# Performance work log

Measured on AMD Instinct MI355X. Metric: run time of the kernel, lower is better.

## Reference

```python
import jax, jax.numpy as jnp
import numpy as np
from math import factorial as _f

MAX_L = 2
NUM_CHANNELS = 64
B, N, C = 4, 1024, 64


def _cg_coeff(l1, m1, l2, m2, L, M):
    # Standard real Clebsch-Gordan coefficient <l1 m1 l2 m2 | L M> (Condon-Shortley)
    if m1 + m2 != M or not (abs(l1 - l2) <= L <= l1 + l2):
        return 0.0
    pre = ((2 * L + 1) * _f(L + l1 - l2) * _f(L - l1 + l2) * _f(l1 + l2 - L) / _f(l1 + l2 + L + 1)) ** 0.5
    pre *= (_f(L + M) * _f(L - M) * _f(l1 - m1) * _f(l1 + m1) * _f(l2 - m2) * _f(l2 + m2)) ** 0.5
    s = 0.0
    for k in range(0, l1 + l2 - L + 1):
        dens = [k, l1 + l2 - L - k, l1 - m1 - k, l2 + m2 - k, L - l2 + m1 + k, L - l1 - m2 + k]
        if any(d < 0 for d in dens):
            continue
        term = (-1.0) ** k
        for d in dens:
            term /= _f(d)
        s += term
    return pre * s


def _cg_tensor(l1, l2, L):
    # dense CG block [2l1+1, 2l2+1, 2L+1]
    T = np.zeros((2 * l1 + 1, 2 * l2 + 1, 2 * L + 1), np.float32)
    for i, m1 in enumerate(range(-l1, l1 + 1)):
        for j, m2 in enumerate(range(-l2, l2 + 1)):
            for k, M in enumerate(range(-L, L + 1)):
                T[i, j, k] = _cg_coeff(l1, m1, l2, m2, L, M)
    return jnp.asarray(T)


# precompute small CG blocks once (tiny, static)
_CG = {(l1, l2, L): _cg_tensor(l1, l2, L)
       for l1 in range(MAX_L + 1) for l2 in range(MAX_L + 1)
       for L in range(MAX_L + 1) if abs(l1 - l2) <= L <= l1 + l2}


def setup_inputs() -> dict:
    key = jax.random.key(0)
    ks = jax.random.split(key, 7)
    inp = {}
    for l, k in zip(range(MAX_L + 1), ks[:3]):
        inp[f"v{l}"] = jax.random.normal(k, (B, N, 2 * l + 1, C), jnp.float32)
    for l, k in zip(range(MAX_L + 1), ks[3:6]):
        inp[f"s{l}"] = jax.random.normal(k, (B, N, N, 2 * l + 1, 1), jnp.float32)
    inp["conn"] = jax.random.randint(ks[6], (B, N, N), 0, 2, jnp.int32)
    return inp


def reference(v0, v1, v2, s0, s1, s2, conn):
    v = [v0, v1, v2]
    sph = [s0, s1, s2]
    # sphx.parts[l] = einsum('bijmc->bimc', sph.parts[l]) : sum over neighbor index j
    sx = [jnp.einsum('bijmc->bimc', s) for s in sph]
    adj = conn.astype(v0.dtype)  # [B,N,N] gather mask (Rmask1)

    # CGproduct(vertices, sphx): for each output degree L, concat all (l1,l2) fragments
    cg_parts = []
    for L in range(MAX_L + 1):
        frags = []
        for l1 in range(MAX_L + 1):
            for l2 in range(MAX_L + 1):
                if abs(l1 - l2) <= L <= l1 + l2:
                    # [B,N,2L+1,C*1]
                    o = jnp.einsum('bnic,bnjd,ijk->bnkcd', v[l1], sx[l2], _CG[(l1, l2, L)])
                    frags.append(o.reshape(o.shape[0], o.shape[1], 2 * L + 1, -1))
        cg_parts.append(jnp.concatenate(frags, axis=-1))

    # message passing: sum-gather over connected neighbors
    mp = [jnp.einsum('bnm,bmkc->bnkc', adj, p) for p in cg_parts]

    # per-l normalization: divide by (2l+1)*||part||_F / num_channels
    normed = []
    for L, p in enumerate(mp):
        nf = (2 * L + 1) * jnp.linalg.norm(p)
        normed.append(p / (nf / NUM_CHANNELS))

    # flatten (m, channel) per degree and concat for a single output array
    return jnp.concatenate([p.reshape(p.shape[0], p.shape[1], -1) for p in normed], axis=-1)
```

## Files before the change

kernel.cpp:

```cpp
#include <hip/hip_runtime.h>
#include <math.h>

typedef __attribute__((ext_vector_type(8))) short short8;
typedef __attribute__((ext_vector_type(4))) float f32x4;

#define B_   4
#define N_   1024
#define FTOT 3264
#define FPAD 3328

#define WS_SS   0
#define WS_CG   256
#define WS_SX   4096
#define WS_ABF  151552
#define WS_PT   8540160

__device__ __forceinline__ unsigned short f2bf(float x) {
  union { float f; unsigned u; } v; v.f = x;
  unsigned r = v.u + 0x7FFFu + ((v.u >> 16) & 1u);
  return (unsigned short)(r >> 16);
}

__device__ __forceinline__ void gload16(const void* gp, void* lp) {
  __builtin_amdgcn_global_load_lds((const __attribute__((address_space(1))) unsigned int*)gp,
                                   (__attribute__((address_space(3))) unsigned int*)lp, 16, 0, 0);
}

__device__ __forceinline__ float wave_sum(float v) {
#pragma unroll
  for (int off = 32; off > 0; off >>= 1) v += __shfl_down(v, off, 64);
  return v;
}

__device__ double dfact(int n) { double r = 1.0; for (int i = 2; i <= n; ++i) r *= (double)i; return r; }

__device__ float cg_coeff(int l1, int m1, int l2, int m2, int L, int M) {
  if (m1 + m2 != M) return 0.f;
  int dl = l1 - l2; if (dl < 0) dl = -dl;
  if (L < dl || L > l1 + l2) return 0.f;
  double pre = sqrt((double)(2*L+1) * dfact(L+l1-l2) * dfact(L-l1+l2) * dfact(l1+l2-L) / dfact(l1+l2+L+1));
  pre *= sqrt(dfact(L+M)*dfact(L-M)*dfact(l1-m1)*dfact(l1+m1)*dfact(l2-m2)*dfact(l2+m2));
  double s = 0.0;
  for (int k = 0; k <= l1 + l2 - L; ++k) {
    int d1 = l1+l2-L-k, d2 = l1-m1-k, d3 = l2+m2-k, d4 = L-l2+m1+k, d5 = L-l1-m2+k;
    if (d1 < 0 || d2 < 0 || d3 < 0 || d4 < 0 || d5 < 0) continue;
    double t = (k & 1) ? -1.0 : 1.0;
    t /= dfact(k)*dfact(d1)*dfact(d2)*dfact(d3)*dfact(d4)*dfact(d5);
    s += t;
  }
  return (float)(pre * s);
}

__device__ const int t_l1[15]  = {0,1,2, 0,1,1,1,2,2, 0,1,1,2,2,2};
__device__ const int t_l2[15]  = {0,1,2, 1,0,1,2,1,2, 2,1,2,0,1,2};
__device__ const int t_L [15]  = {0,0,0, 1,1,1,1,1,1, 2,2,2,2,2,2};
__device__ const int t_off[16] = {0,1,10, 35,44,53,80,125,170, 245,270,315,390,415,490, 615};

__device__ const int d_l1[3][6]  = {{0,1,2,0,0,0},{0,1,1,1,2,2},{0,1,1,2,2,2}};
__device__ const int d_l2[3][6]  = {{0,1,2,0,0,0},{1,0,1,2,1,2},{2,1,2,0,1,2}};
__device__ const int d_off[3][6] = {{0,1,10,0,0,0},{35,44,53,80,125,170},{245,270,315,390,415,490}};
__device__ const int d_rb[3] = {0, 1, 4};

__global__ __launch_bounds__(256) void k_pre(const float* __restrict__ s0p, const float* __restrict__ s1p,
                                             const float* __restrict__ s2p, float* __restrict__ sx,
                                             const int* __restrict__ conn, unsigned short* __restrict__ Abf,
                                             float* __restrict__ ss, float* __restrict__ cg) {
  __shared__ float red[9][256];
  const int tid = threadIdx.x;

  if (blockIdx.x < 4096) {
    const int bn = blockIdx.x;
    const f32x4* p0 = (const f32x4*)(s0p + (size_t)bn * 1024);
    const f32x4* p1 = (const f32x4*)(s1p + (size_t)bn * 3072);
    const f32x4* p2 = (const f32x4*)(s2p + (size_t)bn * 5120);

    f32x4 va = p0[tid];
    f32x4 vb[3];
#pragma unroll
    for (int it = 0; it < 3; ++it) vb[it] = p1[tid + 256 * it];
    f32x4 vc[5];
#pragma unroll
    for (int it = 0; it < 5; ++it) vc[it] = p2[tid + 256 * it];

    float a = va[0] + va[1] + va[2] + va[3];

    float b[3] = {0.f, 0.f, 0.f};
#pragma unroll
    for (int it = 0; it < 3; ++it)
#pragma unroll
      for (int e = 0; e < 4; ++e)
        b[(it + e) % 3] += vb[it][e];

    float c[5] = {0.f, 0.f, 0.f, 0.f, 0.f};
#pragma unroll
    for (int it = 0; it < 5; ++it)
#pragma unroll
      for (int e = 0; e < 4; ++e)
        c[(4 * it + e) % 5] += vc[it][e];

    red[0][tid] = a;
    const int r3 = tid % 3;
#pragma unroll
    for (int u = 0; u < 3; ++u) red[1 + (r3 + u) % 3][tid] = b[u];
    const int q5 = (4 * tid) % 5;
#pragma unroll
    for (int u = 0; u < 5; ++u) red[4 + (q5 + u) % 5][tid] = c[u];
    __syncthreads();

    const int lane = tid & 63, w = tid >> 6;
    for (int r = w; r < 9; r += 4) {
      float v = red[r][lane] + red[r][lane + 64] + red[r][lane + 128] + red[r][lane + 192];
      v = wave_sum(v);
      if (lane == 0) sx[(size_t)bn * 9 + r] = v;
    }
    return;
  }

  const int idx  = (blockIdx.x - 4096) * 256 + tid;
  const int lane = idx & 63;
  const int w    = (idx >> 6) & 2047;
  const int b    = idx >> 17;
  const int nt16 = w >> 5;
  const int ks   = w & 31;
  const int l16  = lane & 15, quad = lane >> 4;
  const int n    = nt16 * 16 + l16;
  const int m8   = ks * 32 + quad * 8;
  const int4* src = (const int4*)(conn + ((size_t)(b * 1024 + n) * 1024 + m8));
  int4 c0 = src[0], c1 = src[1];
  short8 o;
  o[0] = f2bf((float)c0.x); o[1] = f2bf((float)c0.y);
  o[2] = f2bf((float)c0.z); o[3] = f2bf((float)c0.w);
  o[4] = f2bf((float)c1.x); o[5] = f2bf((float)c1.y);
  o[6] = f2bf((float)c1.z); o[7] = f2bf((float)c1.w);
  const int nt = n >> 7, nr = n & 127;
  *(short8*)&Abf[(size_t)(b * 8 + nt) * 131072 + ks * 4096 +
                 ((nr >> 4) * 4 + quad) * 128 + (nr & 15) * 8] = o;

  if (blockIdx.x == 4096) {
    if (tid < 4) ss[tid] = 0.f;
    for (int t0 = tid; t0 < 615; t0 += 256) {
      int t = 0;
      while (t < 14 && t0 >= t_off[t+1]) ++t;
      int local = t0 - t_off[t];
      int l1 = t_l1[t], l2 = t_l2[t], L = t_L[t];
      int nk = 2*L+1, n2 = 2*l2+1;
      int k = local % nk; int rest = local / nk;
      int j = rest % n2;  int i = rest / n2;
      cg[t0] = cg_coeff(l1, i - l1, l2, j - l2, L, k - L);
    }
  }
}

#define VSTRIDE 148

template <int L>
__device__ __forceinline__ void cg_emit(const float* __restrict__ vme, const float sxr[9],
                                        const float* __restrict__ cgt,
                                        unsigned short* __restrict__ pout, int cbase) {
  const int nfrag = (L == 0) ? 3 : 6;
  const int nk = 2 * L + 1;
  const int Lbase = (L == 0) ? 0 : (L == 1 ? 192 : 1344);
  const int Cfrag = nfrag * 64;
#pragma unroll
  for (int frag = 0; frag < nfrag; ++frag) {
    const int l1 = d_l1[L][frag], l2 = d_l2[L][frag];
    const int n1 = 2 * l1 + 1, n2 = 2 * l2 + 1;
    const int rb1 = d_rb[l1], rb2 = d_rb[l2];
    const int cgo = d_off[L][frag];
#pragma unroll
    for (int k = 0; k < nk; ++k) {
      float w[5];
#pragma unroll
      for (int i = 0; i < n1; ++i) {
        float a = 0.f;
#pragma unroll
        for (int j = 0; j < n2; ++j)
          a += sxr[rb2 + j] * cgt[cgo + (i * n2 + j) * nk + k];
        w[i] = a;
      }
      f32x4 val = {0.f, 0.f, 0.f, 0.f};
#pragma unroll
      for (int i = 0; i < n1; ++i) {
        f32x4 vv = *(const f32x4*)(vme + (rb1 + i) * 16);
        val += vv * w[i];
      }
      const int fb = Lbase + k * Cfrag + frag * 64 + cbase;
      const int ftile = fb >> 7, fr = fb & 127;
      unsigned short* pp = pout + (size_t)ftile * 131072 + (fr >> 4) * 512 + (fr & 15) * 8;
#pragma unroll
      for (int cc = 0; cc < 4; ++cc)
        pp[cc * 8] = f2bf(val[cc]);
    }
  }
}

__global__ __launch_bounds__(256) void k_cgp(const float* __restrict__ v0, const float* __restrict__ v1,
                                             const float* __restrict__ v2, const float* __restrict__ sx,
                                             const float* __restrict__ cgt, unsigned short* __restrict__ Pt) {
  __shared__ float vsh[64 * VSTRIDE];
  const int half = blockIdx.x & 1;
  const int cq   = blockIdx.x >> 1;
  const int mt   = blockIdx.y;
  const int b    = blockIdx.z;
  const int m0 = mt * 64;
  const int c0 = cq * 16;
  const int tid = threadIdx.x;
  const size_t nb = (size_t)b * N_ + m0;

  {
    const int mloc = tid >> 2;
    const int cc0  = (tid & 3) * 4;
    const size_t vrow = nb + mloc;
    *(f32x4*)&vsh[mloc*VSTRIDE + 0*16 + cc0] = *(const f32x4*)&v0[vrow * 64 + c0 + cc0];
#pragma unroll
    for (int r = 1; r < 4; ++r)
      *(f32x4*)&vsh[mloc*VSTRIDE + r*16 + cc0] = *(const f32x4*)&v1[(vrow * 3 + (r-1)) * 64 + c0 + cc0];
#pragma unroll
    for (int r = 4; r < 9; ++r)
      *(f32x4*)&vsh[mloc*VSTRIDE + r*16 + cc0] = *(const f32x4*)&v2[(vrow * 5 + (r-4)) * 64 + c0 + cc0];
  }
  const int lane = tid & 63, wv = tid >> 6;
  float sxr[9];
#pragma unroll
  for (int r = 0; r < 9; ++r) sxr[r] = sx[(nb + lane) * 9 + r];
  __syncthreads();

  const int ks = mt * 2 + (lane >> 5);
  const int kq = ((lane & 31) >> 3) * 128 + (lane & 7);
  unsigned short* pout = Pt + (size_t)b * 26 * 131072 + ks * 4096 + kq;
  const int cbase = c0 + wv * 4;
  const float* vme = &vsh[lane * VSTRIDE + wv * 4];

  if (half == 0) {
    cg_emit<0>(vme, sxr, cgt, pout, cbase);
    cg_emit<1>(vme, sxr, cgt, pout, cbase);
  } else {
    cg_emit<2>(vme, sxr, cgt, pout, cbase);
    const int fr = 64 + cbase;
    unsigned short* pp = pout + (size_t)25 * 131072 + (fr >> 4) * 512 + (fr & 15) * 8;
#pragma unroll
    for (int cc = 0; cc < 4; ++cc)
      pp[cc * 8] = 0;
  }
}

#define WAIT_VM8 0x0F78
#define WAIT_VM0 0x0F70
#define NBLK 208

__global__ __launch_bounds__(512, 2) void k_gemm(const unsigned short* __restrict__ PtT,
                                                 const unsigned short* __restrict__ AbT,
                                                 float* __restrict__ out, float* __restrict__ ssv) {
  __shared__ unsigned short As[2][2][8192];
  __shared__ unsigned short Bs[2][2][8192];
  const int i  = blockIdx.x;
  const int x  = i & 7, j = i >> 3;
  const int b   = x >> 1;
  const int ntp = 2 * (x & 1) + (j & 1);
  const int ftp = j >> 1;
  const int f0 = ftp * 256, n0 = ntp * 256;
  const int tid  = threadIdx.x;
  const int w    = tid >> 6, lane = tid & 63;
  const int wr   = w >> 2, wc = w & 3;
  const int l16  = lane & 15, quad = lane >> 4;

  const unsigned short* gA0 = PtT + (size_t)(b * 26 + 2 * ftp    ) * 131072;
  const unsigned short* gA1 = PtT + (size_t)(b * 26 + 2 * ftp + 1) * 131072;
  const unsigned short* gB0 = AbT + (size_t)(b * 8  + 2 * ntp    ) * 131072;
  const unsigned short* gB1 = AbT + (size_t)(b * 8  + 2 * ntp + 1) * 131072;
  const int so = w * 512 + lane * 8;

#define ISSUE(T, BUF) do { \
    const size_t o = (size_t)(T) * 8192 + so; \
    gload16(gA0 + o,        &As[BUF][0][w * 512]); \
    gload16(gA0 + o + 4096, &As[BUF][0][4096 + w * 512]); \
    gload16(gA1 + o,        &As[BUF][1][w * 512]); \
    gload16(gA1 + o + 4096, &As[BUF][1][4096 + w * 512]); \
    gload16(gB0 + o,        &Bs[BUF][0][w * 512]); \
    gload16(gB0 + o + 4096, &Bs[BUF][0][4096 + w * 512]); \
    gload16(gB1 + o,        &Bs[BUF][1][w * 512]); \
    gload16(gB1 + o + 4096, &Bs[BUF][1][4096 + w * 512]); \
  } while (0)

  f32x4 acc[8][4] = {};
  const int bh  = wc >> 1;
  const int bl4 = (wc & 1) * 4;

#define COMPUTE(BUF) do { \
    _Pragma("unroll") \
    for (int kc = 0; kc < 2; ++kc) { \
      short8 bf[4]; \
      _Pragma("unroll") \
      for (int ni = 0; ni < 4; ++ni) \
        bf[ni] = *(const short8*)&Bs[BUF][bh][kc*4096 + ((bl4 + ni)*4 + quad)*128 + l16*8]; \
      _Pragma("unroll") \
      for (int mh = 0; mh < 2; ++mh) { \
        short8 af[4]; \
        _Pragma("unroll") \
        for (int m = 0; m < 4; ++m) \
          af[m] = *(const short8*)&As[BUF][wr][kc*4096 + ((mh*4 + m)*4 + quad)*128 + l16*8]; \
        _Pragma("unroll") \
        for (int m = 0; m < 4; ++m) \
          _Pragma("unroll") \
          for (int ni = 0; ni < 4; ++ni) \
            acc[mh*4 + m][ni] = __builtin_amdgcn_mfma_f32_16x16x32_bf16(af[m], bf[ni], acc[mh*4 + m][ni], 0, 0, 0); \
      } \
    } \
  } while (0)

  ISSUE(0, 0);
  ISSUE(1, 1);
  for (int t = 0; t < 15; ++t) {
    const int buf = t & 1;
    __builtin_amdgcn_s_waitcnt(WAIT_VM8);
    __builtin_amdgcn_s_barrier();
    COMPUTE(buf);
    __builtin_amdgcn_s_barrier();
    if (t < 14) ISSUE(t + 2, buf);
  }
  __builtin_amdgcn_s_waitcnt(WAIT_VM0);
  __builtin_amdgcn_s_barrier();
  COMPUTE(1);

  float ssl0 = 0.f, ssl1 = 0.f, ssl2 = 0.f;
#pragma unroll
  for (int mi = 0; mi < 8; ++mi) {
    const int fbase = f0 + wr*128 + mi*16 + quad*4;
    if (fbase >= FTOT) continue;
    float sq = 0.f;
#pragma unroll
    for (int ni = 0; ni < 4; ++ni) {
      f32x4 v = acc[mi][ni];
      sq += v[0]*v[0] + v[1]*v[1] + v[2]*v[2] + v[3]*v[3];
    }
    if (fbase < 192) ssl0 += sq; else if (fbase < 1344) ssl1 += sq; else ssl2 += sq;
  }
  ssl0 = wave_sum(ssl0); ssl1 = wave_sum(ssl1); ssl2 = wave_sum(ssl2);

  __syncthreads();
  float* red = (float*)&As[0][0][0];
  if (lane == 0) { red[w*3 + 0] = ssl0; red[w*3 + 1] = ssl1; red[w*3 + 2] = ssl2; }
  __syncthreads();
  if (tid < 3) {
    float s = 0.f;
#pragma unroll
    for (int ww = 0; ww < 8; ++ww) s += red[ww*3 + tid];
    if (s != 0.f) atomicAdd(&ssv[tid], s);
  }
  __syncthreads();

  int* cnt = (int*)(ssv + 3);
  if (tid == 0) {
    __threadfence();
    atomicAdd(cnt, 1);
    while (atomicAdd(cnt, 0) < NBLK) __builtin_amdgcn_s_sleep(8);
  }
  __syncthreads();

  if (tid < 3) red[tid] = atomicAdd(&ssv[tid], 0.f);
  __syncthreads();
  const float sc0 = 64.f / (1.f * sqrtf(red[0]));
  const float sc1 = 64.f / (3.f * sqrtf(red[1]));
  const float sc2 = 64.f / (5.f * sqrtf(red[2]));

#pragma unroll
  for (int mi = 0; mi < 8; ++mi) {
    const int fbase = f0 + wr*128 + mi*16 + quad*4;
    if (fbase >= FTOT) continue;
    const float sc = fbase < 192 ? sc0 : (fbase < 1344 ? sc1 : sc2);
#pragma unroll
    for (int ni = 0; ni < 4; ++ni) {
      const int n = n0 + wc*64 + ni*16 + l16;
      f32x4 v = acc[mi][ni];
      v *= sc;
      *(f32x4*)&out[((size_t)b * N_ + n) * FTOT + fbase] = v;
    }
  }
#undef ISSUE
#undef COMPUTE
}

extern "C" void kernel_launch(void* const* d_in, const int* in_sizes, int n_in,
                              void* d_out, int out_size, void* d_ws, size_t ws_size,
                              hipStream_t stream) {
  const float* v0 = (const float*)d_in[0];
  const float* v1 = (const float*)d_in[1];
  const float* v2 = (const float*)d_in[2];
  const float* s0 = (const float*)d_in[3];
  const float* s1 = (const float*)d_in[4];
  const float* s2 = (const float*)d_in[5];
  const int* conn = (const int*)d_in[6];
  char* ws = (char*)d_ws;
  float* ss            = (float*)(ws + WS_SS);
  float* cg            = (float*)(ws + WS_CG);
  float* sx            = (float*)(ws + WS_SX);
  unsigned short* Abf  = (unsigned short*)(ws + WS_ABF);
  unsigned short* Pt   = (unsigned short*)(ws + WS_PT);
  float* out = (float*)d_out;

  k_pre  <<<dim3(6144),         dim3(256), 0, stream>>>(s0, s1, s2, sx, conn, Abf, ss, cg);
  k_cgp  <<<dim3(8, 16, B_),    dim3(256), 0, stream>>>(v0, v1, v2, sx, cg, Pt);
  k_gemm <<<dim3(208),          dim3(512), 0, stream>>>(Pt, Abf, out, ss);
}
```

Measured before the change: 273.3 us.

## Fuse neighbor-sum, CG coefficient and CG product kernels into one front kernel

Merges the s-reduction pre-kernel and the CG-product kernel into a single front kernel. Each block reduces eight rows of spherical inputs into shared memory, with the loads for the next row issued before the current row is reduced, and then computes the CG product for those rows directly. CG coefficients are recomputed per block into LDS instead of going through global workspace. This removes one launch and the global round trip for sx and cg. In exchange, each block recomputes the 615 coefficients with double-precision code, and the reduction becomes a sequential loop with two barriers per row.

```diff
diff --git a/kernel.cpp b/kernel.cpp
--- a/kernel.cpp
+++ b/kernel.cpp
@@ -10,8 +10,6 @@
 #define FPAD 3328
 
 #define WS_SS   0
-#define WS_CG   256
-#define WS_SX   4096
 #define WS_ABF  151552
 #define WS_PT   8540160
 
@@ -61,102 +59,10 @@
 __device__ const int d_off[3][6] = {{0,1,10,0,0,0},{35,44,53,80,125,170},{245,270,315,390,415,490}};
 __device__ const int d_rb[3] = {0, 1, 4};
 
-__global__ __launch_bounds__(256) void k_pre(const float* __restrict__ s0p, const float* __restrict__ s1p,
-                                             const float* __restrict__ s2p, float* __restrict__ sx,
-                                             const int* __restrict__ conn, unsigned short* __restrict__ Abf,
-                                             float* __restrict__ ss, float* __restrict__ cg) {
-  __shared__ float red[9][256];
-  const int tid = threadIdx.x;
-
-  if (blockIdx.x < 4096) {
-    const int bn = blockIdx.x;
-    const f32x4* p0 = (const f32x4*)(s0p + (size_t)bn * 1024);
-    const f32x4* p1 = (const f32x4*)(s1p + (size_t)bn * 3072);
-    const f32x4* p2 = (const f32x4*)(s2p + (size_t)bn * 5120);
-
-    f32x4 va = p0[tid];
-    f32x4 vb[3];
-#pragma unroll
-    for (int it = 0; it < 3; ++it) vb[it] = p1[tid + 256 * it];
-    f32x4 vc[5];
-#pragma unroll
-    for (int it = 0; it < 5; ++it) vc[it] = p2[tid + 256 * it];
-
-    float a = va[0] + va[1] + va[2] + va[3];
-
-    float b[3] = {0.f, 0.f, 0.f};
-#pragma unroll
-    for (int it = 0; it < 3; ++it)
-#pragma unroll
-      for (int e = 0; e < 4; ++e)
-        b[(it + e) % 3] += vb[it][e];
-
-    float c[5] = {0.f, 0.f, 0.f, 0.f, 0.f};
-#pragma unroll
-    for (int it = 0; it < 5; ++it)
-#pragma unroll
-      for (int e = 0; e < 4; ++e)
-        c[(4 * it + e) % 5] += vc[it][e];
-
-    red[0][tid] = a;
-    const int r3 = tid % 3;
-#pragma unroll
-    for (int u = 0; u < 3; ++u) red[1 + (r3 + u) % 3][tid] = b[u];
-    const int q5 = (4 * tid) % 5;
-#pragma unroll
-    for (int u = 0; u < 5; ++u) red[4 + (q5 + u) % 5][tid] = c[u];
-    __syncthreads();
-
-    const int lane = tid & 63, w = tid >> 6;
-    for (int r = w; r < 9; r += 4) {
-      float v = red[r][lane] + red[r][lane + 64] + red[r][lane + 128] + red[r][lane + 192];
-      v = wave_sum(v);
-      if (lane == 0) sx[(size_t)bn * 9 + r] = v;
-    }
-    return;
-  }
-
-  const int idx  = (blockIdx.x - 4096) * 256 + tid;
-  const int lane = idx & 63;
-  const int w    = (idx >> 6) & 2047;
-  const int b    = idx >> 17;
-  const int nt16 = w >> 5;
-  const int ks   = w & 31;
-  const int l16  = lane & 15, quad = lane >> 4;
-  const int n    = nt16 * 16 + l16;
-  const int m8   = ks * 32 + quad * 8;
-  const int4* src = (const int4*)(conn + ((size_t)(b * 1024 + n) * 1024 + m8));
-  int4 c0 = src[0], c1 = src[1];
-  short8 o;
-  o[0] = f2bf((float)c0.x); o[1] = f2bf((float)c0.y);
-  o[2] = f2bf((float)c0.z); o[3] = f2bf((float)c0.w);
-  o[4] = f2bf((float)c1.x); o[5] = f2bf((float)c1.y);
-  o[6] = f2bf((float)c1.z); o[7] = f2bf((float)c1.w);
-  const int nt = n >> 7, nr = n & 127;
-  *(short8*)&Abf[(size_t)(b * 8 + nt) * 131072 + ks * 4096 +
-                 ((nr >> 4) * 4 + quad) * 128 + (nr & 15) * 8] = o;
-
-  if (blockIdx.x == 4096) {
-    if (tid < 4) ss[tid] = 0.f;
-    for (int t0 = tid; t0 < 615; t0 += 256) {
-      int t = 0;
-      while (t < 14 && t0 >= t_off[t+1]) ++t;
-      int local = t0 - t_off[t];
-      int l1 = t_l1[t], l2 = t_l2[t], L = t_L[t];
-      int nk = 2*L+1, n2 = 2*l2+1;
-      int k = local % nk; int rest = local / nk;
-      int j = rest % n2;  int i = rest / n2;
-      cg[t0] = cg_coeff(l1, i - l1, l2, j - l2, L, k - L);
-    }
-  }
-}
-
-#define VSTRIDE 148
-
-template <int L>
-__device__ __forceinline__ void cg_emit(const float* __restrict__ vme, const float sxr[9],
-                                        const float* __restrict__ cgt,
-                                        unsigned short* __restrict__ pout, int cbase) {
+template <int L, int RS>
+__device__ __forceinline__ void cg_emit(const float* vme, const float sxr[9],
+                                        const float* cgt,
+                                        unsigned short* pout, int cbase) {
   const int nfrag = (L == 0) ? 3 : 6;
   const int nk = 2 * L + 1;
   const int Lbase = (L == 0) ? 0 : (L == 1 ? 192 : 1344);
@@ -181,7 +87,7 @@
       f32x4 val = {0.f, 0.f, 0.f, 0.f};
 #pragma unroll
       for (int i = 0; i < n1; ++i) {
-        f32x4 vv = *(const f32x4*)(vme + (rb1 + i) * 16);
+        f32x4 vv = *(const f32x4*)(vme + (rb1 + i) * RS);
         val += vv * w[i];
       }
       const int fb = Lbase + k * Cfrag + frag * 64 + cbase;
@@ -194,53 +100,143 @@
   }
 }
 
-__global__ __launch_bounds__(256) void k_cgp(const float* __restrict__ v0, const float* __restrict__ v1,
-                                             const float* __restrict__ v2, const float* __restrict__ sx,
-                                             const float* __restrict__ cgt, unsigned short* __restrict__ Pt) {
-  __shared__ float vsh[64 * VSTRIDE];
-  const int half = blockIdx.x & 1;
-  const int cq   = blockIdx.x >> 1;
-  const int mt   = blockIdx.y;
-  const int b    = blockIdx.z;
-  const int m0 = mt * 64;
-  const int c0 = cq * 16;
+__global__ __launch_bounds__(256) void k_front(const float* __restrict__ v0, const float* __restrict__ v1,
+                                               const float* __restrict__ v2,
+                                               const float* __restrict__ s0p, const float* __restrict__ s1p,
+                                               const float* __restrict__ s2p,
+                                               const int* __restrict__ conn, unsigned short* __restrict__ Abf,
+                                               unsigned short* __restrict__ Pt, float* __restrict__ ss) {
   const int tid = threadIdx.x;
-  const size_t nb = (size_t)b * N_ + m0;
-
-  {
-    const int mloc = tid >> 2;
-    const int cc0  = (tid & 3) * 4;
-    const size_t vrow = nb + mloc;
-    *(f32x4*)&vsh[mloc*VSTRIDE + 0*16 + cc0] = *(const f32x4*)&v0[vrow * 64 + c0 + cc0];
-#pragma unroll
-    for (int r = 1; r < 4; ++r)
-      *(f32x4*)&vsh[mloc*VSTRIDE + r*16 + cc0] = *(const f32x4*)&v1[(vrow * 3 + (r-1)) * 64 + c0 + cc0];
-#pragma unroll
-    for (int r = 4; r < 9; ++r)
-      *(f32x4*)&vsh[mloc*VSTRIDE + r*16 + cc0] = *(const f32x4*)&v2[(vrow * 5 + (r-4)) * 64 + c0 + cc0];
-  }
+
+  if (blockIdx.x >= 512) {
+    const int idx  = (blockIdx.x - 512) * 256 + tid;
+    const int lane = idx & 63;
+    const int w    = (idx >> 6) & 2047;
+    const int b    = idx >> 17;
+    const int nt16 = w >> 5;
+    const int ks   = w & 31;
+    const int l16  = lane & 15, quad = lane >> 4;
+    const int n    = nt16 * 16 + l16;
+    const int m8   = ks * 32 + quad * 8;
+    const int4* src = (const int4*)(conn + ((size_t)(b * 1024 + n) * 1024 + m8));
+    int4 c0 = src[0], c1 = src[1];
+    short8 o;
+    o[0] = f2bf((float)c0.x); o[1] = f2bf((float)c0.y);
+    o[2] = f2bf((float)c0.z); o[3] = f2bf((float)c0.w);
+    o[4] = f2bf((float)c1.x); o[5] = f2bf((float)c1.y);
+    o[6] = f2bf((float)c1.z); o[7] = f2bf((float)c1.w);
+    const int nt = n >> 7, nr = n & 127;
+    *(short8*)&Abf[(size_t)(b * 8 + nt) * 131072 + ks * 4096 +
+                   ((nr >> 4) * 4 + quad) * 128 + (nr & 15) * 8] = o;
+    if (blockIdx.x == 512 && tid < 4) ss[tid] = 0.f;
+    return;
+  }
+
+  __shared__ float cgl[616];
+  __shared__ float vsh[8 * 580];
+  __shared__ float red[9][256];
+  __shared__ float sxl[8][12];
+
+  const int b   = blockIdx.x >> 7;
+  const int mt8 = blockIdx.x & 127;
+  const int n0g = mt8 * 8;
+  const size_t nb = (size_t)b * N_ + n0g;
+
+  f32x4 va, vb[3], vc[5];
+#define SX_LOAD(RR) do { \
+    const f32x4* p0 = (const f32x4*)(s0p + (nb + (RR)) * 1024); \
+    const f32x4* p1 = (const f32x4*)(s1p + (nb + (RR)) * 3072); \
+    const f32x4* p2 = (const f32x4*)(s2p + (nb + (RR)) * 5120); \
+    va = p0[tid]; \
+    _Pragma("unroll") for (int it = 0; it < 3; ++it) vb[it] = p1[tid + 256 * it]; \
+    _Pragma("unroll") for (int it = 0; it < 5; ++it) vc[it] = p2[tid + 256 * it]; \
+  } while (0)
+
+  SX_LOAD(0);
+
+  for (int t0 = tid; t0 < 615; t0 += 256) {
+    int t = 0;
+    while (t < 14 && t0 >= t_off[t+1]) ++t;
+    int local = t0 - t_off[t];
+    int l1 = t_l1[t], l2 = t_l2[t], L = t_L[t];
+    int nk = 2*L+1, n2 = 2*l2+1;
+    int k = local % nk; int rest = local / nk;
+    int j = rest % n2;  int i = rest / n2;
+    cgl[t0] = cg_coeff(l1, i - l1, l2, j - l2, L, k - L);
+  }
+
   const int lane = tid & 63, wv = tid >> 6;
+  const int r3 = tid % 3;
+  const int q5 = (4 * tid) % 5;
+
+  for (int r = 0; r < 8; ++r) {
+    float a = va[0] + va[1] + va[2] + va[3];
+    float bb[3] = {0.f, 0.f, 0.f};
+#pragma unroll
+    for (int it = 0; it < 3; ++it)
+#pragma unroll
+      for (int e = 0; e < 4; ++e)
+        bb[(it + e) % 3] += vb[it][e];
+    float cc[5] = {0.f, 0.f, 0.f, 0.f, 0.f};
+#pragma unroll
+    for (int it = 0; it < 5; ++it)
+#pragma unroll
+      for (int e = 0; e < 4; ++e)
+        cc[(4 * it + e) % 5] += vc[it][e];
+
+    if (r < 7) SX_LOAD(r + 1);
+
+    red[0][tid] = a;
+#pragma unroll
+    for (int u = 0; u < 3; ++u) red[1 + (r3 + u) % 3][tid] = bb[u];
+#pragma unroll
+    for (int u = 0; u < 5; ++u) red[4 + (q5 + u) % 5][tid] = cc[u];
+    __syncthreads();
+
+    for (int rr = wv; rr < 9; rr += 4) {
+      float v = red[rr][lane] + red[rr][lane + 64] + red[rr][lane + 128] + red[rr][lane + 192];
+      v = wave_sum(v);
+      if (lane == 0) sxl[r][rr] = v;
+    }
+    __syncthreads();
+  }
+#undef SX_LOAD
+
+  for (int e = tid; e < 1152; e += 256) {
+    const int m = e / 144, rest = e % 144;
+    const int rr = rest >> 4, c4 = (rest & 15) * 4;
+    const size_t vrow = nb + m;
+    f32x4 val;
+    if (rr == 0)      val = *(const f32x4*)&v0[vrow * 64 + c4];
+    else if (rr < 4)  val = *(const f32x4*)&v1[(vrow * 3 + (rr - 1)) * 64 + c4];
+    else              val = *(const f32x4*)&v2[(vrow * 5 + (rr - 4)) * 64 + c4];
+    *(f32x4*)&vsh[m * 580 + rr * 64 + c4] = val;
+  }
+  __syncthreads();
+
+  const int m  = tid & 7;
+  const int cq = (tid >> 3) & 15;
+  const int half = tid >> 7;
+  const int mg = n0g + m;
+  const int ks = mg >> 5;
+  const int kq = ((mg & 31) >> 3) * 128 + (mg & 7);
+  unsigned short* pout = Pt + (size_t)b * 26 * 131072 + ks * 4096 + kq;
+  const int cbase = cq * 4;
   float sxr[9];
 #pragma unroll
-  for (int r = 0; r < 9; ++r) sxr[r] = sx[(nb + lane) * 9 + r];
-  __syncthreads();
-
-  const int ks = mt * 2 + (lane >> 5);
-  const int kq = ((lane & 31) >> 3) * 128 + (lane & 7);
-  unsigned short* pout = Pt + (size_t)b * 26 * 131072 + ks * 4096 + kq;
-  const int cbase = c0 + wv * 4;
-  const float* vme = &vsh[lane * VSTRIDE + wv * 4];
+  for (int rr = 0; rr < 9; ++rr) sxr[rr] = sxl[m][rr];
+  const float* vme = &vsh[m * 580 + cbase];
 
   if (half == 0) {
-    cg_emit<0>(vme, sxr, cgt, pout, cbase);
-    cg_emit<1>(vme, sxr, cgt, pout, cbase);
+    cg_emit<0, 64>(vme, sxr, cgl, pout, cbase);
+    cg_emit<1, 64>(vme, sxr, cgl, pout, cbase);
   } else {
-    cg_emit<2>(vme, sxr, cgt, pout, cbase);
+    cg_emit<2, 64>(vme, sxr, cgl, pout, cbase);
     const int fr = 64 + cbase;
     unsigned short* pp = pout + (size_t)25 * 131072 + (fr >> 4) * 512 + (fr & 15) * 8;
 #pragma unroll
-    for (int cc = 0; cc < 4; ++cc)
-      pp[cc * 8] = 0;
+    for (int c2 = 0; c2 < 4; ++c2)
+      pp[c2 * 8] = 0;
   }
 }
 
@@ -392,13 +388,10 @@
   const int* conn = (const int*)d_in[6];
   char* ws = (char*)d_ws;
   float* ss            = (float*)(ws + WS_SS);
-  float* cg            = (float*)(ws + WS_CG);
-  float* sx            = (float*)(ws + WS_SX);
   unsigned short* Abf  = (unsigned short*)(ws + WS_ABF);
   unsigned short* Pt   = (unsigned short*)(ws + WS_PT);
   float* out = (float*)d_out;
 
-  k_pre  <<<dim3(6144),         dim3(256), 0, stream>>>(s0, s1, s2, sx, conn, Abf, ss, cg);
-  k_cgp  <<<dim3(8, 16, B_),    dim3(256), 0, stream>>>(v0, v1, v2, sx, cg, Pt);
-  k_gemm <<<dim3(208),          dim3(512), 0, stream>>>(Pt, Abf, out, ss);
-}
+  k_front<<<dim3(2560), dim3(256), 0, stream>>>(v0, v1, v2, s0, s1, s2, conn, Abf, Pt, ss);
+  k_gemm <<<dim3(208),  dim3(512), 0, stream>>>(Pt, Abf, out, ss);
+}
```

Result: no change. 273.8 us (+0.2%).
